# Kernel optimization log

Measured on AMD Instinct MI355X. Metric: run time of the kernel, lower is better.

Reference implementation:

```python
import jax, jax.numpy as jnp
import numpy as np

BLOCK_SIZE = 32
HEADS = 8
DIM_HEAD = 64
ROPE_THETA = 10000.0


def rmsnorm(x, w):
    eps = jnp.finfo(x.dtype).eps
    var = jnp.mean(jnp.square(x), axis=-1, keepdims=True)
    return x * jax.lax.rsqrt(var + eps) * w


def rope_cos_sin(seq_len, dim_head):
    # lucidrains rotary-embedding-torch default: interleaved pairs, theta=10000
    inv_freq = 1.0 / (ROPE_THETA ** (jnp.arange(0, dim_head, 2, dtype=jnp.float32) / dim_head))
    freqs = jnp.arange(seq_len, dtype=jnp.float32)[:, None] * inv_freq[None, :]  # [S, Dh/2]
    return jnp.cos(freqs), jnp.sin(freqs)


def apply_rope(t, cos, sin):
    # t: [B, H, S, Dh], cos/sin: [S, Dh/2]
    t1 = t[..., 0::2]
    t2 = t[..., 1::2]
    out = jnp.stack([t1 * cos - t2 * sin, t1 * sin + t2 * cos], axis=-1)
    return out.reshape(t.shape)


def split_heads(x, h):
    b, n, _ = x.shape
    return x.reshape(b, n, h, -1).transpose(0, 2, 1, 3)  # b h n d


def forward(tokens, attn_norm_w, qkv_w, out_w, mix_w, mix_b,
            ff_norm_w, ff_in_w, ff_in_b, ff_out_w, ff_out_b, final_norm_w):
    B, S, D = tokens.shape
    L = qkv_w.shape[0]
    H, Dh = HEADS, DIM_HEAD
    scale = Dh ** -0.5
    cos, sin = rope_cos_sin(S, Dh)

    # block-causal mask: q_idx // block >= kv_idx // block
    idx = jnp.arange(S)
    allowed = (idx[:, None] // BLOCK_SIZE) >= (idx[None, :] // BLOCK_SIZE)  # [S, S] bool
    neg = -jnp.finfo(tokens.dtype).max

    t = tokens
    first_v = None
    for l in range(L):
        # --- block causal attention ---
        x = rmsnorm(t, attn_norm_w[l])
        qkv = x @ qkv_w[l]  # [B, S, 3*H*Dh]
        q, k, v = jnp.split(qkv, 3, axis=-1)
        q, k, v = split_heads(q, H), split_heads(k, H), split_heads(v, H)  # b h s d
        orig_v = v
        if l > 0:
            mix = jax.nn.sigmoid(x @ mix_w[l] + mix_b[l])  # [B, S, H]
            mix = mix.transpose(0, 2, 1)[..., None]  # [B, H, S, 1]
            v = v + mix * (first_v - v)  # lerp
        q = apply_rope(q, cos, sin)
        k = apply_rope(k, cos, sin)
        sim = jnp.einsum('bhid,bhjd->bhij', q * scale, k)
        sim = jnp.where(allowed, sim, neg)
        attn = jax.nn.softmax(sim, axis=-1)
        o = jnp.einsum('bhij,bhjd->bhid', attn, v)
        o = o.transpose(0, 2, 1, 3).reshape(B, S, H * Dh)
        t = t + o @ out_w[l]
        if first_v is None:
            first_v = orig_v
        # --- SwiGLU feedforward ---
        y = rmsnorm(t, ff_norm_w[l])
        h = y @ ff_in_w[l] + ff_in_b[l]
        a, g = jnp.split(h, 2, axis=-1)
        y = (a * jax.nn.gelu(g, approximate=False)) @ ff_out_w[l] + ff_out_b[l]
        t = t + y

    return rmsnorm(t, final_norm_w)


def setup_inputs():
    key = jax.random.key(0)
    B, S, D, L = 2, 2048, 512, 4
    Di = HEADS * DIM_HEAD  # 512
    Dhid = int(D * 4.0 * 2 / 3)  # 1365
    ks = jax.random.split(key, 8)
    s = 0.02
    return {
        'tokens': jax.random.normal(ks[0], (B, S, D), jnp.float32),
        'attn_norm_w': jnp.ones((L, D), jnp.float32),
        'qkv_w': jax.random.normal(ks[1], (L, D, 3 * Di), jnp.float32) * s,
        'out_w': jax.random.normal(ks[2], (L, Di, D), jnp.float32) * s,
        'mix_w': jax.random.normal(ks[3], (L, D, HEADS), jnp.float32) * s,
        'mix_b': jnp.zeros((L, HEADS), jnp.float32),
        'ff_norm_w': jnp.ones((L, D), jnp.float32),
        'ff_in_w': jax.random.normal(ks[4], (L, D, 2 * Dhid), jnp.float32) * s,
        'ff_in_b': jnp.zeros((L, 2 * Dhid), jnp.float32),
        'ff_out_w': jax.random.normal(ks[5], (L, Dhid, D), jnp.float32) * s,
        'ff_out_b': jnp.zeros((L, D), jnp.float32),
        'final_norm_w': jnp.ones((D,), jnp.float32),
    }


def reference(tokens, attn_norm_w, qkv_w, out_w, mix_w, mix_b,
              ff_norm_w, ff_in_w, ff_in_b, ff_out_w, ff_out_b, final_norm_w):
    return forward(tokens, attn_norm_w, qkv_w, out_w, mix_w, mix_b,
                   ff_norm_w, ff_in_w, ff_in_b, ff_out_w, ff_out_b, final_norm_w)
```

## Files before the change

kernel.cpp:

```cpp
#include <hip/hip_runtime.h>
#include <hip/hip_bf16.h>
#include <math.h>

typedef __bf16 bf16;
typedef bf16 bf16x8 __attribute__((ext_vector_type(8)));
typedef float f32x4 __attribute__((ext_vector_type(4)));

#define LDS16(gp, lp) __builtin_amdgcn_global_load_lds( \
    (const __attribute__((address_space(1))) unsigned int*)(gp), \
    (__attribute__((address_space(3))) unsigned int*)(lp), 16, 0, 0)

__device__ __forceinline__ int cumoff2(int qtp) {
  if (qtp < 4)  return qtp;
  if (qtp < 8)  return 4 + 2 * (qtp - 4);
  if (qtp < 12) return 12 + 3 * (qtp - 8);
  return 24 + 4 * (qtp - 12);
}

__global__ void convert_w_kernel(const float* __restrict__ W, bf16* __restrict__ WT,
                                 int K, int N, int Kp, int Np,
                                 size_t wstride, size_t wtstride)
{
  __shared__ float tile[32][33];
  const float* Wl = W + blockIdx.z * wstride;
  bf16* WTl = WT + blockIdx.z * wtstride;
  int k0 = blockIdx.x * 32, n0 = blockIdx.y * 32;
  int tx = threadIdx.x, ty = threadIdx.y;
  for (int i = ty; i < 32; i += 8) {
    int k = k0 + i, n = n0 + tx;
    tile[i][tx] = (k < K && n < N) ? Wl[(size_t)k * N + n] : 0.f;
  }
  __syncthreads();
  for (int i = ty; i < 32; i += 8) {
    int n = n0 + i, k = k0 + tx;
    if (n < Np && k < Kp) WTl[(size_t)n * Kp + k] = (bf16)tile[tx][i];
  }
}

__global__ __launch_bounds__(256)
void rope_kernel(float* __restrict__ tab)
{
  int idx = blockIdx.x * 256 + threadIdx.x;
  int s = idx >> 5, j = idx & 31;
  float invf = (float)exp((double)(2 * j) * -0.14391156847064293);
  float ang = (float)s * invf;
  float sn, cs;
  sincosf(ang, &sn, &cs);
  tab[idx] = cs;
  tab[65536 + idx] = sn;
}

template<bool BF16OUT>
__global__ __launch_bounds__(64)
void rmsnorm_kernel(const float* __restrict__ in, const float* __restrict__ wgt,
                    void* __restrict__ outp)
{
  int row = blockIdx.x, lane = threadIdx.x;
  const float* p = in + (size_t)row * 512;
  float4 v0 = *(const float4*)(p + lane * 4);
  float4 v1 = *(const float4*)(p + 256 + lane * 4);
  float ss = v0.x*v0.x + v0.y*v0.y + v0.z*v0.z + v0.w*v0.w
           + v1.x*v1.x + v1.y*v1.y + v1.z*v1.z + v1.w*v1.w;
  #pragma unroll
  for (int d = 1; d < 64; d <<= 1) ss += __shfl_xor(ss, d);
  float sc = rsqrtf(ss * (1.f / 512.f) + 1.1920929e-7f);
  float a0[4] = {v0.x, v0.y, v0.z, v0.w};
  float a1[4] = {v1.x, v1.y, v1.z, v1.w};
  #pragma unroll
  for (int i = 0; i < 4; ++i) {
    int c0 = lane * 4 + i, c1 = 256 + lane * 4 + i;
    float r0 = a0[i] * sc * wgt[c0];
    float r1 = a1[i] * sc * wgt[c1];
    if (BF16OUT) {
      ((bf16*)outp)[(size_t)row * 512 + c0] = (bf16)r0;
      ((bf16*)outp)[(size_t)row * 512 + c1] = (bf16)r1;
    } else {
      ((float*)outp)[(size_t)row * 512 + c0] = r0;
      ((float*)outp)[(size_t)row * 512 + c1] = r1;
    }
  }
}

__global__ __launch_bounds__(256)
void qkvpost_kernel(const bf16* __restrict__ qkv, const float* __restrict__ mb,
                    const float* __restrict__ rope, float* __restrict__ firstv,
                    bf16* __restrict__ qb, bf16* __restrict__ kb,
                    bf16* __restrict__ vT, int layer)
{
  int idx = blockIdx.x * 256 + threadIdx.x;
  int j = idx & 31;
  int s = (idx >> 5) & 2047;
  int bh = idx >> 16;
  int b = bh >> 3, h = bh & 7;
  size_t row = (size_t)b * 2048 + s;
  const bf16* base = qkv + row * 1664 + h * 64 + 2 * j;
  float q1 = (float)base[0],    q2 = (float)base[1];
  float k1 = (float)base[512],  k2 = (float)base[513];
  float v1 = (float)base[1024], v2 = (float)base[1025];
  float cs = rope[s * 32 + j];
  float sn = rope[65536 + s * 32 + j];
  size_t qoff = ((size_t)bh * 2048 + s) * 64 + 2 * j;
  qb[qoff]     = (bf16)((q1 * cs - q2 * sn) * 0.125f);
  qb[qoff + 1] = (bf16)((q1 * sn + q2 * cs) * 0.125f);
  kb[qoff]     = (bf16)(k1 * cs - k2 * sn);
  kb[qoff + 1] = (bf16)(k1 * sn + k2 * cs);
  if (layer == 0) {
    firstv[qoff] = v1; firstv[qoff + 1] = v2;
  } else {
    float logit = (float)qkv[row * 1664 + 1536 + h] + mb[h];
    float mx = 1.f / (1.f + __expf(-logit));
    v1 += mx * (firstv[qoff] - v1);
    v2 += mx * (firstv[qoff + 1] - v2);
  }
  vT[((size_t)bh * 64 + 2 * j) * 2048 + s]     = (bf16)v1;
  vT[((size_t)bh * 64 + 2 * j + 1) * 2048 + s] = (bf16)v2;
}

__global__ __launch_bounds__(256, 3)
void attn_kernel(const bf16* __restrict__ Q, const bf16* __restrict__ Kmat,
                 const bf16* __restrict__ VT, float* __restrict__ Opart,
                 float* __restrict__ lbuf)
{
  __shared__ __align__(16) bf16 smK[2][8 * 512];
  __shared__ __align__(16) bf16 smV[2][8 * 512];
  __shared__ __align__(16) bf16 smP[4][2][16 * 72];
  const int bid = blockIdx.x;
  const int bh = bid & 15;
  const int cidx = bid >> 4;
  int qtp, chunk;
  if (cidx < 4)       { qtp = cidx; chunk = 0; }
  else if (cidx < 12) { qtp = 4 + ((cidx - 4) >> 1);  chunk = (cidx - 4) & 1; }
  else if (cidx < 24) { int t = cidx - 12; qtp = 8 + t / 3; chunk = t - (qtp - 8) * 3; }
  else                { int t = cidx - 24; qtp = 12 + (t >> 2); chunk = t & 3; }
  const int jt0 = chunk * 8;
  const int njt = min(jt0 + 8, 2 * qtp + 2) - jt0;

  const int tid = threadIdx.x;
  const int w = tid >> 6, lane = tid & 63;
  const int c = lane & 15, quad = lane >> 4;
  const int jtmax_w = (qtp * 4 + w) >> 1;

  const size_t qrow0 = (size_t)bh * 2048 + qtp * 128 + w * 32;
  bf16x8 aQ[2][2];
  #pragma unroll
  for (int m = 0; m < 2; ++m) {
    aQ[m][0] = *(const bf16x8*)(Q + (qrow0 + m * 16 + c) * 64 + quad * 8);
    aQ[m][1] = *(const bf16x8*)(Q + (qrow0 + m * 16 + c) * 64 + 32 + quad * 8);
  }

  const bf16* Kg = Kmat + ((size_t)bh * 2048 + w * 16 + c) * 64 + quad * 8;
  const bf16* Vg = VT + ((size_t)bh * 64 + w * 16 + c) * 2048 + quad * 8;

  {
    const bf16* kp = Kg + (size_t)jt0 * 4096;
    const bf16* vp = Vg + jt0 * 64;
    LDS16(kp,      smK[0] + w * 1024);
    LDS16(kp + 32, smK[0] + w * 1024 + 512);
    LDS16(vp,      smV[0] + w * 1024);
    LDS16(vp + 32, smV[0] + w * 1024 + 512);
  }

  f32x4 o[2][4] = {};
  float lacc[2][4] = {};

  for (int j = 0; j < njt; ++j) {
    const int b = j & 1;
    const int jt = jt0 + j;
    __syncthreads();
    if (j + 1 < njt) {
      const bf16* kp = Kg + (size_t)(jt + 1) * 4096;
      const bf16* vp = Vg + (jt + 1) * 64;
      bf16* kd = smK[1 - b] + w * 1024;
      bf16* vd = smV[1 - b] + w * 1024;
      LDS16(kp,      kd);
      LDS16(kp + 32, kd + 512);
      LDS16(vp,      vd);
      LDS16(vp + 32, vd + 512);
    }
    if (jt > jtmax_w) continue;

    f32x4 s[2][4];
    #pragma unroll
    for (int nt = 0; nt < 4; ++nt) {
      bf16x8 bK0 = *(const bf16x8*)(smK[b] + (nt * 2) * 512 + lane * 8);
      bf16x8 bK1 = *(const bf16x8*)(smK[b] + (nt * 2 + 1) * 512 + lane * 8);
      #pragma unroll
      for (int m = 0; m < 2; ++m) {
        f32x4 acc = {0.f, 0.f, 0.f, 0.f};
        acc = __builtin_amdgcn_mfma_f32_16x16x32_bf16(aQ[m][0], bK0, acc, 0, 0, 0);
        acc = __builtin_amdgcn_mfma_f32_16x16x32_bf16(aQ[m][1], bK1, acc, 0, 0, 0);
        s[m][nt] = acc;
      }
    }
    if (2 * jt + 1 > 4 * qtp + w) {
      #pragma unroll
      for (int m = 0; m < 2; ++m)
        #pragma unroll
        for (int r = 0; r < 4; ++r) { s[m][2][r] = -3.0e38f; s[m][3][r] = -3.0e38f; }
    }

    #pragma unroll
    for (int m = 0; m < 2; ++m) {
      #pragma unroll
      for (int r = 0; r < 4; ++r) {
        float p0 = __expf(s[m][0][r]);
        float p1 = __expf(s[m][1][r]);
        float p2 = __expf(s[m][2][r]);
        float p3 = __expf(s[m][3][r]);
        lacc[m][r] += (p0 + p1) + (p2 + p3);
        bf16* pp = smP[w][m] + (quad * 4 + r) * 72 + c;
        pp[0]  = (bf16)p0;
        pp[16] = (bf16)p1;
        pp[32] = (bf16)p2;
        pp[48] = (bf16)p3;
      }
    }
    asm volatile("s_waitcnt lgkmcnt(0)" ::: "memory");

    #pragma unroll
    for (int ks2 = 0; ks2 < 2; ++ks2) {
      #pragma unroll
      for (int m = 0; m < 2; ++m) {
        bf16x8 aP = *(const bf16x8*)(smP[w][m] + c * 72 + ks2 * 32 + quad * 8);
        #pragma unroll
        for (int nt = 0; nt < 4; ++nt) {
          bf16x8 bV = *(const bf16x8*)(smV[b] + (nt * 2 + ks2) * 512 + lane * 8);
          o[m][nt] = __builtin_amdgcn_mfma_f32_16x16x32_bf16(aP, bV, o[m][nt], 0, 0, 0);
        }
      }
    }
  }

  #pragma unroll
  for (int m = 0; m < 2; ++m)
    #pragma unroll
    for (int r = 0; r < 4; ++r) {
      float v = lacc[m][r];
      #pragma unroll
      for (int d = 1; d < 16; d <<= 1) v += __shfl_xor(v, d);
      lacc[m][r] = v;
    }

  const int slot = bh * 40 + cumoff2(qtp) + chunk;
  float* Op = Opart + (size_t)slot * 8192;
  #pragma unroll
  for (int m = 0; m < 2; ++m) {
    #pragma unroll
    for (int r = 0; r < 4; ++r) {
      int prow = w * 32 + m * 16 + quad * 4 + r;
      #pragma unroll
      for (int nt = 0; nt < 4; ++nt)
        Op[prow * 64 + nt * 16 + c] = o[m][nt][r];
      if (c == 0) lbuf[slot * 128 + prow] = lacc[m][r];
    }
  }
}

__global__ __launch_bounds__(256)
void attn_combine_kernel(const float* __restrict__ Opart, const float* __restrict__ lbuf,
                         bf16* __restrict__ Omat)
{
  const int qt = blockIdx.x, bh = blockIdx.y;
  const int qtp = qt >> 1;
  const int nch = (2 * qtp + 9) >> 3;
  const int base = bh * 40 + cumoff2(qtp);
  const int tid = threadIdx.x;
  const int row = tid >> 2, cg = tid & 3;
  const int prow = (qt & 1) * 64 + row;

  float L = 0.f;
  f32x4 acc[4] = {{0,0,0,0},{0,0,0,0},{0,0,0,0},{0,0,0,0}};
  #pragma unroll
  for (int ch = 0; ch < 4; ++ch) {
    if (ch < nch) {
      L += lbuf[(base + ch) * 128 + prow];
      const f32x4* p = (const f32x4*)(Opart + (size_t)(base + ch) * 8192 + prow * 64 + cg * 16);
      #pragma unroll
      for (int i = 0; i < 4; ++i) acc[i] += p[i];
    }
  }
  float inv = 1.f / L;

  const int b = bh >> 3, h = bh & 7;
  bf16* op = Omat + ((size_t)b * 2048 + qt * 64 + row) * 512 + h * 64 + cg * 16;
  #pragma unroll
  for (int i = 0; i < 4; ++i)
    #pragma unroll
    for (int j = 0; j < 4; ++j)
      op[i * 4 + j] = (bf16)(acc[i][j] * inv);
}

template<int MODE>
__global__ __launch_bounds__(256, 2)
void gemm_kernel(const bf16* __restrict__ A, const bf16* __restrict__ WT,
                 const float* __restrict__ bias, int n_bias,
                 const float* __restrict__ Tin, void* __restrict__ outp,
                 int K, int N)
{
  __shared__ __align__(16) bf16 smA[8 * 512];
  __shared__ __align__(16) bf16 smB[8 * 512];
  const int tid = threadIdx.x;
  const int w = tid >> 6, lane = tid & 63;
  const int c = lane & 15, quad = lane >> 4;
  const int wy = w >> 1, wx = w & 1;
  const int bm = blockIdx.y * 128, bn = blockIdx.x * 128;

  f32x4 acc[4][4] = {};

  const bf16* Ag0 = A  + (size_t)(bm + (w * 2)     * 16 + c) * K + quad * 8;
  const bf16* Ag1 = A  + (size_t)(bm + (w * 2 + 1) * 16 + c) * K + quad * 8;
  const bf16* Bg0 = WT + (size_t)(bn + (w * 2)     * 16 + c) * K + quad * 8;
  const bf16* Bg1 = WT + (size_t)(bn + (w * 2 + 1) * 16 + c) * K + quad * 8;
  bf16* la0 = smA + (w * 2) * 512;
  bf16* la1 = smA + (w * 2 + 1) * 512;
  bf16* lb0 = smB + (w * 2) * 512;
  bf16* lb1 = smB + (w * 2 + 1) * 512;

  const int NK = K >> 5;
  for (int kk = 0; kk < NK; ++kk) {
    const int ko = kk * 32;
    LDS16(Ag0 + ko, la0);
    LDS16(Ag1 + ko, la1);
    LDS16(Bg0 + ko, lb0);
    LDS16(Bg1 + ko, lb1);
    __syncthreads();
    bf16x8 af[4], bfr[4];
    #pragma unroll
    for (int mt = 0; mt < 4; ++mt)
      af[mt] = *(const bf16x8*)(smA + (wy * 4 + mt) * 512 + lane * 8);
    #pragma unroll
    for (int nt = 0; nt < 4; ++nt)
      bfr[nt] = *(const bf16x8*)(smB + (wx * 4 + nt) * 512 + lane * 8);
    #pragma unroll
    for (int mt = 0; mt < 4; ++mt)
      #pragma unroll
      for (int nt = 0; nt < 4; ++nt)
        acc[mt][nt] = __builtin_amdgcn_mfma_f32_16x16x32_bf16(af[mt], bfr[nt], acc[mt][nt], 0, 0, 0);
    __syncthreads();
  }

  const int r0 = bm + wy * 64;
  const int c0 = bn + wx * 64;
  #pragma unroll
  for (int mt = 0; mt < 4; ++mt) {
    #pragma unroll
    for (int nt = 0; nt < 4; ++nt) {
      #pragma unroll
      for (int r = 0; r < 4; ++r) {
        size_t row = (size_t)(r0 + mt * 16 + quad * 4 + r);
        int col = c0 + nt * 16 + c;
        float v = acc[mt][nt][r];
        float bv = (bias != nullptr && col < n_bias) ? bias[col] : 0.f;
        if (MODE == 2) {
          ((float*)outp)[row * N + col] = Tin[row * N + col] + v + bv;
        } else if (MODE == 1) {
          ((float*)outp)[row * N + col] = v;
        } else {
          ((bf16*)outp)[row * N + col] = (bf16)(v + bv);
        }
      }
    }
  }
}

template<int MODE>
__global__ __launch_bounds__(256, 4)
void gemm64_kernel(const bf16* __restrict__ A, const bf16* __restrict__ WT,
                   const float* __restrict__ bias, int n_bias,
                   const float* __restrict__ Tin, void* __restrict__ outp,
                   int K, int N)
{
  __shared__ __align__(16) bf16 smA[4 * 512];
  __shared__ __align__(16) bf16 smB[4 * 512];
  const int tid = threadIdx.x;
  const int w = tid >> 6, lane = tid & 63;
  const int c = lane & 15, quad = lane >> 4;
  const int wy = w >> 1, wx = w & 1;
  const int bm = blockIdx.y * 64, bn = blockIdx.x * 64;

  f32x4 acc[2][2] = {};

  const bf16* Ag = A  + (size_t)(bm + w * 16 + c) * K + quad * 8;
  const bf16* Bg = WT + (size_t)(bn + w * 16 + c) * K + quad * 8;
  bf16* la = smA + w * 512;
  bf16* lb = smB + w * 512;

  const int NK = K >> 5;
  for (int kk = 0; kk < NK; ++kk) {
    const int ko = kk * 32;
    LDS16(Ag + ko, la);
    LDS16(Bg + ko, lb);
    __syncthreads();
    bf16x8 af[2], bfr[2];
    #pragma unroll
    for (int mt = 0; mt < 2; ++mt)
      af[mt] = *(const bf16x8*)(smA + (wy * 2 + mt) * 512 + lane * 8);
    #pragma unroll
    for (int nt = 0; nt < 2; ++nt)
      bfr[nt] = *(const bf16x8*)(smB + (wx * 2 + nt) * 512 + lane * 8);
    #pragma unroll
    for (int mt = 0; mt < 2; ++mt)
      #pragma unroll
      for (int nt = 0; nt < 2; ++nt)
        acc[mt][nt] = __builtin_amdgcn_mfma_f32_16x16x32_bf16(af[mt], bfr[nt], acc[mt][nt], 0, 0, 0);
    __syncthreads();
  }

  const int r0 = bm + wy * 32;
  const int c0 = bn + wx * 32;
  #pragma unroll
  for (int mt = 0; mt < 2; ++mt) {
    #pragma unroll
    for (int nt = 0; nt < 2; ++nt) {
      #pragma unroll
      for (int r = 0; r < 4; ++r) {
        size_t row = (size_t)(r0 + mt * 16 + quad * 4 + r);
        int col = c0 + nt * 16 + c;
        float v = acc[mt][nt][r];
        float bv = (bias != nullptr && col < n_bias) ? bias[col] : 0.f;
        if (MODE == 2) {
          ((float*)outp)[row * N + col] = Tin[row * N + col] + v + bv;
        } else if (MODE == 1) {
          ((float*)outp)[row * N + col] = v;
        } else {
          ((bf16*)outp)[row * N + col] = (bf16)(v + bv);
        }
      }
    }
  }
}

__global__ __launch_bounds__(256)
void act_kernel(const bf16* __restrict__ h, bf16* __restrict__ act)
{
  int col = blockIdx.x * 256 + threadIdx.x;
  int row = blockIdx.y;
  if (col >= 1376) return;
  float v = 0.f;
  if (col < 1365) {
    float a = (float)h[(size_t)row * 2816 + col];
    float g = (float)h[(size_t)row * 2816 + 1365 + col];
    v = a * 0.5f * g * (1.f + erff(g * 0.70710678118654752f));
  }
  act[(size_t)row * 1376 + col] = (bf16)v;
}

extern "C" void kernel_launch(void* const* d_in, const int* in_sizes, int n_in,
                              void* d_out, int out_size, void* d_ws, size_t ws_size,
                              hipStream_t stream)
{
  const float* tokens  = (const float*)d_in[0];
  const float* anw     = (const float*)d_in[1];
  const float* qkvw    = (const float*)d_in[2];
  const float* outw    = (const float*)d_in[3];
  const float* mixw    = (const float*)d_in[4];
  const float* mixbias = (const float*)d_in[5];
  const float* fnw     = (const float*)d_in[6];
  const float* ffiw    = (const float*)d_in[7];
  const float* ffib    = (const float*)d_in[8];
  const float* ffow    = (const float*)d_in[9];
  const float* ffob    = (const float*)d_in[10];
  const float* finw    = (const float*)d_in[11];
  float* outp = (float*)d_out;

  char* ws = (char*)d_ws;
  size_t off = 0;
  auto alloc = [&](size_t bytes) -> char* {
    char* p = ws + off;
    off += (bytes + 255) & ~(size_t)255;
    return p;
  };
  bf16* wtq    = (bf16*)alloc((size_t)4 * 1664 * 512 * 2);
  bf16* wto    = (bf16*)alloc((size_t)4 * 512 * 512 * 2);
  bf16* wtfi   = (bf16*)alloc((size_t)4 * 2816 * 512 * 2);
  bf16* wtfo   = (bf16*)alloc((size_t)4 * 512 * 1376 * 2);
  float* tbuf  = (float*)alloc((size_t)4096 * 512 * 4);
  bf16* xb     = (bf16*)alloc((size_t)4096 * 512 * 2);
  bf16* yb     = (bf16*)alloc((size_t)4096 * 512 * 2);
  char* qkvraw = alloc((size_t)4096 * 1664 * 4);
  float* fv    = (float*)alloc((size_t)16 * 2048 * 64 * 4);
  bf16* qb     = (bf16*)alloc((size_t)16 * 2048 * 64 * 2);
  bf16* kbuf   = (bf16*)alloc((size_t)16 * 2048 * 64 * 2);
  bf16* vT     = (bf16*)alloc((size_t)16 * 2048 * 64 * 2);
  bf16* ob     = (bf16*)alloc((size_t)4096 * 512 * 2);
  bf16* hb     = (bf16*)alloc((size_t)4096 * 2816 * 2);
  bf16* actb   = (bf16*)alloc((size_t)4096 * 1376 * 2);
  float* rope  = (float*)alloc((size_t)2 * 65536 * 4);
  float* lbuf  = (float*)alloc((size_t)640 * 128 * 4);
  bf16* qkvbf  = (bf16*)qkvraw;
  float* Opart = (float*)qkvraw;

  dim3 tcv(32, 8);
  convert_w_kernel<<<dim3(16, 48, 4), tcv, 0, stream>>>(
      qkvw, wtq, 512, 1536, 512, 1536, (size_t)512 * 1536, (size_t)1664 * 512);
  convert_w_kernel<<<dim3(16, 4, 4), tcv, 0, stream>>>(
      mixw, wtq + (size_t)1536 * 512, 512, 8, 512, 128, (size_t)512 * 8, (size_t)1664 * 512);
  convert_w_kernel<<<dim3(16, 16, 4), tcv, 0, stream>>>(
      outw, wto, 512, 512, 512, 512, (size_t)512 * 512, (size_t)512 * 512);
  convert_w_kernel<<<dim3(16, 88, 4), tcv, 0, stream>>>(
      ffiw, wtfi, 512, 2730, 512, 2816, (size_t)512 * 2730, (size_t)2816 * 512);
  convert_w_kernel<<<dim3(43, 16, 4), tcv, 0, stream>>>(
      ffow, wtfo, 1365, 512, 1376, 512, (size_t)1365 * 512, (size_t)1376 * 512);
  rope_kernel<<<256, 256, 0, stream>>>(rope);
  hipMemcpyAsync(tbuf, tokens, (size_t)4096 * 512 * 4, hipMemcpyDeviceToDevice, stream);

  for (int l = 0; l < 4; ++l) {
    rmsnorm_kernel<true><<<4096, 64, 0, stream>>>(tbuf, anw + l * 512, xb);
    gemm_kernel<0><<<dim3(13, 32), 256, 0, stream>>>(
        xb, wtq + (size_t)l * 1664 * 512, nullptr, 0, nullptr, qkvbf, 512, 1664);
    qkvpost_kernel<<<4096, 256, 0, stream>>>(qkvbf, mixbias + l * 8, rope, fv, qb, kbuf, vT, l);
    attn_kernel<<<640, 256, 0, stream>>>(qb, kbuf, vT, Opart, lbuf);
    attn_combine_kernel<<<dim3(32, 16), 256, 0, stream>>>(Opart, lbuf, ob);
    gemm64_kernel<2><<<dim3(8, 64), 256, 0, stream>>>(
        ob, wto + (size_t)l * 512 * 512, nullptr, 0, tbuf, tbuf, 512, 512);
    rmsnorm_kernel<true><<<4096, 64, 0, stream>>>(tbuf, fnw + l * 512, yb);
    gemm_kernel<0><<<dim3(22, 32), 256, 0, stream>>>(
        yb, wtfi + (size_t)l * 2816 * 512, ffib + (size_t)l * 2730, 2730, nullptr, hb, 512, 2816);
    act_kernel<<<dim3(6, 4096), 256, 0, stream>>>(hb, actb);
    gemm64_kernel<2><<<dim3(8, 64), 256, 0, stream>>>(
        actb, wtfo + (size_t)l * 512 * 1376, ffob + (size_t)l * 512, 512, tbuf, tbuf, 1376, 512);
  }
  rmsnorm_kernel<false><<<4096, 64, 0, stream>>>(tbuf, finw, outp);
}
```

Measured before the change: 816.6 us.

## Fuse GEGLU into FF-in GEMM epilogue via interleaved weights; shrink buffers to bf16

The FF-in weight columns and bias are interleaved so each value/gate pair sits in adjacent output columns. The GEMM epilogue then computes the GELU-gated product with a lane shuffle and writes the activation directly, which removes the separate activation kernel and the round trip of the hidden buffer. Attention partial outputs and the first-layer V cache are stored in bf16 instead of fp32 to cut memory traffic, at some cost in precision. RMSNorm now packs four rows per 256-thread block to reduce the block count.

```diff
diff --git a/kernel.cpp b/kernel.cpp
--- a/kernel.cpp
+++ b/kernel.cpp
@@ -37,6 +37,36 @@
   }
 }
 
+__global__ void convert_w_ffin_kernel(const float* __restrict__ W, bf16* __restrict__ WT)
+{
+  __shared__ float tile[32][33];
+  const float* Wl = W + (size_t)blockIdx.z * 512 * 2730;
+  bf16* WTl = WT + (size_t)blockIdx.z * 2816 * 512;
+  int k0 = blockIdx.x * 32, n0 = blockIdx.y * 32;
+  int tx = threadIdx.x, ty = threadIdx.y;
+  for (int i = ty; i < 32; i += 8) {
+    int k = k0 + i, n = n0 + tx;
+    int pair = n >> 1;
+    int col = (n & 1) ? 1365 + pair : pair;
+    tile[i][tx] = (pair < 1365) ? Wl[(size_t)k * 2730 + col] : 0.f;
+  }
+  __syncthreads();
+  for (int i = ty; i < 32; i += 8) {
+    int n = n0 + i, k = k0 + tx;
+    WTl[(size_t)n * 512 + k] = (bf16)tile[tx][i];
+  }
+}
+
+__global__ __launch_bounds__(256)
+void ibias_kernel(const float* __restrict__ ffib, float* __restrict__ ib)
+{
+  int idx = blockIdx.x * 256 + threadIdx.x;
+  int l = idx / 2816, n = idx - l * 2816;
+  int pair = n >> 1;
+  int col = (n & 1) ? 1365 + pair : pair;
+  ib[idx] = (pair < 1365) ? ffib[l * 2730 + col] : 0.f;
+}
+
 __global__ __launch_bounds__(256)
 void rope_kernel(float* __restrict__ tab)
 {
@@ -51,11 +81,12 @@
 }
 
 template<bool BF16OUT>
-__global__ __launch_bounds__(64)
+__global__ __launch_bounds__(256)
 void rmsnorm_kernel(const float* __restrict__ in, const float* __restrict__ wgt,
                     void* __restrict__ outp)
 {
-  int row = blockIdx.x, lane = threadIdx.x;
+  int row = blockIdx.x * 4 + (threadIdx.x >> 6);
+  int lane = threadIdx.x & 63;
   const float* p = in + (size_t)row * 512;
   float4 v0 = *(const float4*)(p + lane * 4);
   float4 v1 = *(const float4*)(p + 256 + lane * 4);
@@ -83,7 +114,7 @@
 
 __global__ __launch_bounds__(256)
 void qkvpost_kernel(const bf16* __restrict__ qkv, const float* __restrict__ mb,
-                    const float* __restrict__ rope, float* __restrict__ firstv,
+                    const float* __restrict__ rope, bf16* __restrict__ firstv,
                     bf16* __restrict__ qb, bf16* __restrict__ kb,
                     bf16* __restrict__ vT, int layer)
 {
@@ -105,12 +136,12 @@
   kb[qoff]     = (bf16)(k1 * cs - k2 * sn);
   kb[qoff + 1] = (bf16)(k1 * sn + k2 * cs);
   if (layer == 0) {
-    firstv[qoff] = v1; firstv[qoff + 1] = v2;
+    firstv[qoff] = (bf16)v1; firstv[qoff + 1] = (bf16)v2;
   } else {
     float logit = (float)qkv[row * 1664 + 1536 + h] + mb[h];
     float mx = 1.f / (1.f + __expf(-logit));
-    v1 += mx * (firstv[qoff] - v1);
-    v2 += mx * (firstv[qoff + 1] - v2);
+    v1 += mx * ((float)firstv[qoff] - v1);
+    v2 += mx * ((float)firstv[qoff + 1] - v2);
   }
   vT[((size_t)bh * 64 + 2 * j) * 2048 + s]     = (bf16)v1;
   vT[((size_t)bh * 64 + 2 * j + 1) * 2048 + s] = (bf16)v2;
@@ -118,7 +149,7 @@
 
 __global__ __launch_bounds__(256, 3)
 void attn_kernel(const bf16* __restrict__ Q, const bf16* __restrict__ Kmat,
-                 const bf16* __restrict__ VT, float* __restrict__ Opart,
+                 const bf16* __restrict__ VT, bf16* __restrict__ Opart,
                  float* __restrict__ lbuf)
 {
   __shared__ __align__(16) bf16 smK[2][8 * 512];
@@ -242,7 +273,7 @@
     }
 
   const int slot = bh * 40 + cumoff2(qtp) + chunk;
-  float* Op = Opart + (size_t)slot * 8192;
+  bf16* Op = Opart + (size_t)slot * 8192;
   #pragma unroll
   for (int m = 0; m < 2; ++m) {
     #pragma unroll
@@ -250,14 +281,14 @@
       int prow = w * 32 + m * 16 + quad * 4 + r;
       #pragma unroll
       for (int nt = 0; nt < 4; ++nt)
-        Op[prow * 64 + nt * 16 + c] = o[m][nt][r];
+        Op[prow * 64 + nt * 16 + c] = (bf16)o[m][nt][r];
       if (c == 0) lbuf[slot * 128 + prow] = lacc[m][r];
     }
   }
 }
 
 __global__ __launch_bounds__(256)
-void attn_combine_kernel(const float* __restrict__ Opart, const float* __restrict__ lbuf,
+void attn_combine_kernel(const bf16* __restrict__ Opart, const float* __restrict__ lbuf,
                          bf16* __restrict__ Omat)
 {
   const int qt = blockIdx.x, bh = blockIdx.y;
@@ -269,14 +300,16 @@
   const int prow = (qt & 1) * 64 + row;
 
   float L = 0.f;
-  f32x4 acc[4] = {{0,0,0,0},{0,0,0,0},{0,0,0,0},{0,0,0,0}};
+  float acc[16] = {};
   #pragma unroll
   for (int ch = 0; ch < 4; ++ch) {
     if (ch < nch) {
       L += lbuf[(base + ch) * 128 + prow];
-      const f32x4* p = (const f32x4*)(Opart + (size_t)(base + ch) * 8192 + prow * 64 + cg * 16);
-      #pragma unroll
-      for (int i = 0; i < 4; ++i) acc[i] += p[i];
+      const bf16* p = Opart + (size_t)(base + ch) * 8192 + prow * 64 + cg * 16;
+      bf16x8 u0 = *(const bf16x8*)(p);
+      bf16x8 u1 = *(const bf16x8*)(p + 8);
+      #pragma unroll
+      for (int i = 0; i < 8; ++i) { acc[i] += (float)u0[i]; acc[8 + i] += (float)u1[i]; }
     }
   }
   float inv = 1.f / L;
@@ -284,10 +317,8 @@
   const int b = bh >> 3, h = bh & 7;
   bf16* op = Omat + ((size_t)b * 2048 + qt * 64 + row) * 512 + h * 64 + cg * 16;
   #pragma unroll
-  for (int i = 0; i < 4; ++i)
-    #pragma unroll
-    for (int j = 0; j < 4; ++j)
-      op[i * 4 + j] = (bf16)(acc[i][j] * inv);
+  for (int i = 0; i < 16; ++i)
+    op[i] = (bf16)(acc[i] * inv);
 }
 
 template<int MODE>
@@ -350,13 +381,20 @@
         size_t row = (size_t)(r0 + mt * 16 + quad * 4 + r);
         int col = c0 + nt * 16 + c;
         float v = acc[mt][nt][r];
-        float bv = (bias != nullptr && col < n_bias) ? bias[col] : 0.f;
-        if (MODE == 2) {
-          ((float*)outp)[row * N + col] = Tin[row * N + col] + v + bv;
-        } else if (MODE == 1) {
-          ((float*)outp)[row * N + col] = v;
+        if (MODE == 3) {
+          v += bias[col];
+          float g = __shfl_xor(v, 1);
+          if ((c & 1) == 0) {
+            float outv = v * 0.5f * g * (1.f + erff(g * 0.70710678118654752f));
+            ((bf16*)outp)[row * (size_t)(N >> 1) + (col >> 1)] = (bf16)outv;
+          }
         } else {
-          ((bf16*)outp)[row * N + col] = (bf16)(v + bv);
+          float bv = (bias != nullptr && col < n_bias) ? bias[col] : 0.f;
+          if (MODE == 2) {
+            ((float*)outp)[row * N + col] = Tin[row * N + col] + v + bv;
+          } else {
+            ((bf16*)outp)[row * N + col] = (bf16)(v + bv);
+          }
         }
       }
     }
@@ -420,29 +458,12 @@
         float bv = (bias != nullptr && col < n_bias) ? bias[col] : 0.f;
         if (MODE == 2) {
           ((float*)outp)[row * N + col] = Tin[row * N + col] + v + bv;
-        } else if (MODE == 1) {
-          ((float*)outp)[row * N + col] = v;
         } else {
           ((bf16*)outp)[row * N + col] = (bf16)(v + bv);
         }
       }
     }
   }
-}
-
-__global__ __launch_bounds__(256)
-void act_kernel(const bf16* __restrict__ h, bf16* __restrict__ act)
-{
-  int col = blockIdx.x * 256 + threadIdx.x;
-  int row = blockIdx.y;
-  if (col >= 1376) return;
-  float v = 0.f;
-  if (col < 1365) {
-    float a = (float)h[(size_t)row * 2816 + col];
-    float g = (float)h[(size_t)row * 2816 + 1365 + col];
-    v = a * 0.5f * g * (1.f + erff(g * 0.70710678118654752f));
-  }
-  act[(size_t)row * 1376 + col] = (bf16)v;
 }
 
 extern "C" void kernel_launch(void* const* d_in, const int* in_sizes, int n_in,
@@ -473,22 +494,22 @@
   bf16* wtq    = (bf16*)alloc((size_t)4 * 1664 * 512 * 2);
   bf16* wto    = (bf16*)alloc((size_t)4 * 512 * 512 * 2);
   bf16* wtfi   = (bf16*)alloc((size_t)4 * 2816 * 512 * 2);
-  bf16* wtfo   = (bf16*)alloc((size_t)4 * 512 * 1376 * 2);
+  bf16* wtfo   = (bf16*)alloc((size_t)4 * 512 * 1408 * 2);
+  float* ibias = (float*)alloc((size_t)4 * 2816 * 4);
   float* tbuf  = (float*)alloc((size_t)4096 * 512 * 4);
   bf16* xb     = (bf16*)alloc((size_t)4096 * 512 * 2);
   bf16* yb     = (bf16*)alloc((size_t)4096 * 512 * 2);
-  char* qkvraw = alloc((size_t)4096 * 1664 * 4);
-  float* fv    = (float*)alloc((size_t)16 * 2048 * 64 * 4);
+  char* qkvraw = alloc((size_t)4096 * 1664 * 2);
+  bf16* fv     = (bf16*)alloc((size_t)16 * 2048 * 64 * 2);
   bf16* qb     = (bf16*)alloc((size_t)16 * 2048 * 64 * 2);
   bf16* kbuf   = (bf16*)alloc((size_t)16 * 2048 * 64 * 2);
   bf16* vT     = (bf16*)alloc((size_t)16 * 2048 * 64 * 2);
   bf16* ob     = (bf16*)alloc((size_t)4096 * 512 * 2);
-  bf16* hb     = (bf16*)alloc((size_t)4096 * 2816 * 2);
-  bf16* actb   = (bf16*)alloc((size_t)4096 * 1376 * 2);
+  bf16* actb   = (bf16*)alloc((size_t)4096 * 1408 * 2);
   float* rope  = (float*)alloc((size_t)2 * 65536 * 4);
   float* lbuf  = (float*)alloc((size_t)640 * 128 * 4);
   bf16* qkvbf  = (bf16*)qkvraw;
-  float* Opart = (float*)qkvraw;
+  bf16* Opart  = (bf16*)qkvraw;
 
   dim3 tcv(32, 8);
   convert_w_kernel<<<dim3(16, 48, 4), tcv, 0, stream>>>(
@@ -497,15 +518,15 @@
       mixw, wtq + (size_t)1536 * 512, 512, 8, 512, 128, (size_t)512 * 8, (size_t)1664 * 512);
   convert_w_kernel<<<dim3(16, 16, 4), tcv, 0, stream>>>(
       outw, wto, 512, 512, 512, 512, (size_t)512 * 512, (size_t)512 * 512);
-  convert_w_kernel<<<dim3(16, 88, 4), tcv, 0, stream>>>(
-      ffiw, wtfi, 512, 2730, 512, 2816, (size_t)512 * 2730, (size_t)2816 * 512);
-  convert_w_kernel<<<dim3(43, 16, 4), tcv, 0, stream>>>(
-      ffow, wtfo, 1365, 512, 1376, 512, (size_t)1365 * 512, (size_t)1376 * 512);
+  convert_w_ffin_kernel<<<dim3(16, 88, 4), tcv, 0, stream>>>(ffiw, wtfi);
+  convert_w_kernel<<<dim3(44, 16, 4), tcv, 0, stream>>>(
+      ffow, wtfo, 1365, 512, 1408, 512, (size_t)1365 * 512, (size_t)1408 * 512);
+  ibias_kernel<<<44, 256, 0, stream>>>(ffib, ibias);
   rope_kernel<<<256, 256, 0, stream>>>(rope);
   hipMemcpyAsync(tbuf, tokens, (size_t)4096 * 512 * 4, hipMemcpyDeviceToDevice, stream);
 
   for (int l = 0; l < 4; ++l) {
-    rmsnorm_kernel<true><<<4096, 64, 0, stream>>>(tbuf, anw + l * 512, xb);
+    rmsnorm_kernel<true><<<1024, 256, 0, stream>>>(tbuf, anw + l * 512, xb);
     gemm_kernel<0><<<dim3(13, 32), 256, 0, stream>>>(
         xb, wtq + (size_t)l * 1664 * 512, nullptr, 0, nullptr, qkvbf, 512, 1664);
     qkvpost_kernel<<<4096, 256, 0, stream>>>(qkvbf, mixbias + l * 8, rope, fv, qb, kbuf, vT, l);
@@ -513,12 +534,11 @@
     attn_combine_kernel<<<dim3(32, 16), 256, 0, stream>>>(Opart, lbuf, ob);
     gemm64_kernel<2><<<dim3(8, 64), 256, 0, stream>>>(
         ob, wto + (size_t)l * 512 * 512, nullptr, 0, tbuf, tbuf, 512, 512);
-    rmsnorm_kernel<true><<<4096, 64, 0, stream>>>(tbuf, fnw + l * 512, yb);
-    gemm_kernel<0><<<dim3(22, 32), 256, 0, stream>>>(
-        yb, wtfi + (size_t)l * 2816 * 512, ffib + (size_t)l * 2730, 2730, nullptr, hb, 512, 2816);
-    act_kernel<<<dim3(6, 4096), 256, 0, stream>>>(hb, actb);
+    rmsnorm_kernel<true><<<1024, 256, 0, stream>>>(tbuf, fnw + l * 512, yb);
+    gemm_kernel<3><<<dim3(22, 32), 256, 0, stream>>>(
+        yb, wtfi + (size_t)l * 2816 * 512, ibias + (size_t)l * 2816, 2816, nullptr, actb, 512, 2816);
     gemm64_kernel<2><<<dim3(8, 64), 256, 0, stream>>>(
-        actb, wtfo + (size_t)l * 512 * 1376, ffob + (size_t)l * 512, 512, tbuf, tbuf, 1376, 512);
-  }
-  rmsnorm_kernel<false><<<4096, 64, 0, stream>>>(tbuf, finw, outp);
-}
+        actb, wtfo + (size_t)l * 512 * 1408, ffob + (size_t)l * 512, 512, tbuf, tbuf, 1408, 512);
+  }
+  rmsnorm_kernel<false><<<1024, 256, 0, stream>>>(tbuf, finw, outp);
+}
```

Measured after the change: 759.0 us. 1.08x faster.
